# Kernel tuning notes

Measured on AMD Instinct MI355X. Metric: run time of the kernel, lower is better.

Reference implementation:

```python
import jax, jax.numpy as jnp
import numpy as np

EPS = 1e-5  # torch LayerNorm default
H = 8       # heads_num


def _ln(t, g, b):
    m = jnp.mean(t, axis=-1, keepdims=True)
    v = jnp.var(t, axis=-1, keepdims=True)
    return (t - m) / jnp.sqrt(v + EPS) * g + b


def setup_inputs() -> dict:
    key = jax.random.key(0)
    ks = jax.random.split(key, 12)
    B, S, Dq, Dk, Dff = 4, 2048, 512, 768, 2048
    def w(k, shape, scale=0.02):
        return jax.random.normal(k, shape, jnp.float32) * scale
    return {
        "x": jax.random.normal(ks[0], (B, S, Dq), jnp.float32),
        "y": jax.random.normal(ks[1], (B, S, Dk), jnp.float32),
        # cross-attention projections (stored [in, out]; linear_q/k/v have no bias)
        "Wq": w(ks[2], (Dq, Dq)), "Wk": w(ks[3], (Dk, Dq)), "Wv": w(ks[4], (Dk, Dq)),
        "Wo": w(ks[5], (Dq, Dq)), "bo": jnp.zeros((Dq,), jnp.float32),
        # nn.MultiheadAttention packed in-projection and out-projection
        "mha_w_in": w(ks[6], (Dq, 3 * Dq)), "mha_b_in": jnp.zeros((3 * Dq,), jnp.float32),
        "mha_wo": w(ks[7], (Dq, Dq)), "mha_bo": jnp.zeros((Dq,), jnp.float32),
        # 4 LayerNorms
        "ln1_g": jnp.ones((Dq,), jnp.float32), "ln1_b": jnp.zeros((Dq,), jnp.float32),
        "ln2_g": jnp.ones((Dk,), jnp.float32), "ln2_b": jnp.zeros((Dk,), jnp.float32),
        "ln3_g": jnp.ones((Dq,), jnp.float32), "ln3_b": jnp.zeros((Dq,), jnp.float32),
        "ln4_g": jnp.ones((Dq,), jnp.float32), "ln4_b": jnp.zeros((Dq,), jnp.float32),
        # dense MLP (moe=False branch)
        "mlp_w1": w(ks[8], (Dq, Dff)), "mlp_b1": jnp.zeros((Dff,), jnp.float32),
        "mlp_w2": w(ks[9], (Dff, Dq)), "mlp_b2": jnp.zeros((Dq,), jnp.float32),
    }


def reference(x, y, Wq, Wk, Wv, Wo, bo, mha_w_in, mha_b_in, mha_wo, mha_bo,
              ln1_g, ln1_b, ln2_g, ln2_b, ln3_g, ln3_b, ln4_g, ln4_b,
              mlp_w1, mlp_b1, mlp_w2, mlp_b2):
    B, S, D = x.shape
    hd = D // H
    inv_sqrt_hd = 1.0 / np.sqrt(hd).astype(np.float32)

    xn = _ln(x, ln1_g, ln1_b)
    yn = _ln(y, ln2_g, ln2_b)

    # ---- Multi_CrossAttention: manual QK^T softmax V over true seq axis ----
    q = (xn @ Wq).reshape(B, S, H, hd)
    k = (yn @ Wk).reshape(B, -1, H, hd)
    v = (yn @ Wv).reshape(B, -1, H, hd)
    scores = jnp.einsum('bqhd,bkhd->bhqk', q, k) * inv_sqrt_hd  # [B,H,S,S] (512 MB)
    attn = jax.nn.softmax(scores, axis=-1)
    ctx = jnp.einsum('bhqk,bkhd->bqhd', attn, v).reshape(B, S, D)
    ca = ctx @ Wo + bo

    h = _ln(ca + xn, ln3_g, ln3_b)

    # ---- nn.MultiheadAttention (batch_first=False!): axis 0 is the sequence ----
    qkv = h @ mha_w_in + mha_b_in  # [L=B, N=S, 3D]
    q2, k2, v2 = jnp.split(qkv, 3, axis=-1)
    L, N = q2.shape[0], q2.shape[1]
    q2 = q2.reshape(L, N, H, hd)
    k2 = k2.reshape(L, N, H, hd)
    v2 = v2.reshape(L, N, H, hd)
    s2 = jnp.einsum('lnhd,mnhd->nhlm', q2, k2) * inv_sqrt_hd  # [N,H,L,L]
    a2 = jax.nn.softmax(s2, axis=-1)
    sa = jnp.einsum('nhlm,mnhd->lnhd', a2, v2).reshape(L, N, D) @ mha_wo + mha_bo

    h2 = _ln(sa + h, ln4_g, ln4_b)

    # ---- dense MLP (GELU exact, dropout=0) ----
    mlp = jax.nn.gelu(h2 @ mlp_w1 + mlp_b1, approximate=False) @ mlp_w2 + mlp_b2
    return mlp + h2
```

## Files before the change

kernel.cpp:

```cpp
#include <hip/hip_runtime.h>
#include <math.h>

typedef unsigned short u16;
typedef __attribute__((ext_vector_type(8))) short bf8;
typedef __attribute__((ext_vector_type(4))) float f4;
typedef __attribute__((ext_vector_type(4))) unsigned int u32x4;
typedef __attribute__((ext_vector_type(2))) unsigned int u32x2;
typedef __attribute__((ext_vector_type(4))) unsigned short u16x4;
typedef __attribute__((ext_vector_type(8))) unsigned short u16x8;

__device__ __forceinline__ float bf2f(u16 a){
  unsigned u = ((unsigned)a) << 16;
  float f; __builtin_memcpy(&f, &u, 4);
  return f;
}
__device__ __forceinline__ u16 f2bf(float f){
  unsigned u; __builtin_memcpy(&u, &f, 4);
  u += 0x7fffu + ((u >> 16) & 1u);
  return (u16)(u >> 16);
}
__device__ __forceinline__ unsigned packbf(float a, float b){
  unsigned ua, ub;
  __builtin_memcpy(&ua, &a, 4); __builtin_memcpy(&ub, &b, 4);
  ua += 0x8000u; ub += 0x8000u;
  return __builtin_amdgcn_perm(ub, ua, 0x07060302u);
}
__device__ __forceinline__ void gload16(const u16* g, u16* l){
  __builtin_amdgcn_global_load_lds((const __attribute__((address_space(1))) void*)g,
                                   (__attribute__((address_space(3))) void*)l, 16, 0, 0);
}
__device__ __forceinline__ int xcd_swizzle(int orig, int nwg){
  const int qq = nwg >> 3, rr = nwg & 7;
  const int xcd = orig & 7, loc = orig >> 3;
  return (xcd < rr ? xcd * (qq + 1) : rr * (qq + 1) + (xcd - rr) * qq) + loc;
}

__global__ void k_transpose_all(
    const float* __restrict__ Wq, const float* __restrict__ Wk,
    const float* __restrict__ Wv, const float* __restrict__ Wo,
    const float* __restrict__ Win, const float* __restrict__ Wmo,
    const float* __restrict__ W1, const float* __restrict__ W2,
    u16* __restrict__ WqT, u16* __restrict__ WkT, u16* __restrict__ WvT,
    u16* __restrict__ WoT, u16* __restrict__ WinT, u16* __restrict__ WmoT,
    u16* __restrict__ W1T, u16* __restrict__ W2T)
{
  __shared__ float tile[32][33];
  const int tid = blockIdx.x;
  const float* in; u16* out; int R, C, lo;
  if (tid < 1280){
    if (tid < 256)       { in = Wq;  out = WqT;  R = 512; C = 512;  lo = 0; }
    else if (tid < 640)  { in = Wk;  out = WkT;  R = 768; C = 512;  lo = 256; }
    else if (tid < 1024) { in = Wv;  out = WvT;  R = 768; C = 512;  lo = 640; }
    else                 { in = Wo;  out = WoT;  R = 512; C = 512;  lo = 1024; }
  } else {
    if (tid < 2048)      { in = Win; out = WinT; R = 512; C = 1536; lo = 1280; }
    else if (tid < 2304) { in = Wmo; out = WmoT; R = 512; C = 512;  lo = 2048; }
    else if (tid < 3328) { in = W1;  out = W1T;  R = 512; C = 2048; lo = 2304; }
    else                 { in = W2;  out = W2T;  R = 2048; C = 512; lo = 3328; }
  }
  const int local = tid - lo;
  const int tpx = C >> 5;
  const int bx = (local % tpx) * 32, by = (local / tpx) * 32;
  const int tx = threadIdx.x, ty = threadIdx.y;
#pragma unroll
  for (int i = 0; i < 4; i++)
    tile[ty + i*8][tx] = in[(size_t)(by + ty + i*8) * C + bx + tx];
  __syncthreads();
#pragma unroll
  for (int i = 0; i < 4; i++)
    out[(size_t)(bx + ty + i*8) * R + by + tx] = f2bf(tile[tx][ty + i*8]);
}

__global__ __launch_bounds__(256) void k_layernorm(
    const float* __restrict__ in, const float* __restrict__ gam,
    const float* __restrict__ bet, float* __restrict__ outf,
    u16* __restrict__ outb, int D)
{
  const int row = blockIdx.x, t = threadIdx.x;
  const int nv = D >> 8;
  const float* r = in + (size_t)row * D;
  float v[3] = {0.f, 0.f, 0.f};
  float s = 0.f, s2 = 0.f;
#pragma unroll
  for (int i = 0; i < 3; i++){
    if (i < nv){ float xx = r[t + i*256]; v[i] = xx; s += xx; s2 += xx*xx; }
  }
#pragma unroll
  for (int m = 32; m; m >>= 1){ s += __shfl_xor(s, m); s2 += __shfl_xor(s2, m); }
  __shared__ float rs[4], rq[4];
  const int wave = t >> 6;
  if ((t & 63) == 0){ rs[wave] = s; rq[wave] = s2; }
  __syncthreads();
  s  = rs[0] + rs[1] + rs[2] + rs[3];
  s2 = rq[0] + rq[1] + rq[2] + rq[3];
  const float mean = s / (float)D;
  const float var  = s2 / (float)D - mean * mean;
  const float rstd = rsqrtf(var + 1e-5f);
#pragma unroll
  for (int i = 0; i < 3; i++){
    if (i < nv){
      const int c = t + i*256;
      float o = (v[i] - mean) * rstd * gam[c] + bet[c];
      if (outf) outf[(size_t)row * D + c] = o;
      outb[(size_t)row * D + c] = f2bf(o);
    }
  }
}

template<int TM, int TN, bool BIAS, bool RES, bool GELU_ACT, int OUTM>
__global__ __launch_bounds__(256, 4) void k_gemm(
    const u16* __restrict__ A, const u16* __restrict__ BT,
    const float* __restrict__ bias, const float* __restrict__ res,
    float* __restrict__ outf, u16* __restrict__ outb,
    int M, int N, int K)
{
  constexpr int MF = TM / 32;
  constexpr int NF = TN / 32;
  constexpr int WM = TM / 2;
  constexpr int WN = TN / 2;
  __shared__ u16 Sb[(TM + TN) * 64];
  const int t = threadIdx.x;
  const int gx = gridDim.x;
  const int swz = xcd_swizzle(blockIdx.y * gx + blockIdx.x, gx * gridDim.y);
  const int m0 = (swz / gx) * TM, n0 = (swz % gx) * TN;
  const int wave = t >> 6, lane = t & 63;
  const int wm = wave >> 1, wn = wave & 1;
  const int l15 = lane & 15, lg = lane >> 4;
  const u16* Ag = A + (size_t)m0 * K;
  const u16* Bg = BT + (size_t)n0 * K;

  const int lrow = lane >> 3;
  const int csrc = (((lane & 7) ^ lrow) << 3);
  const u16* Agl = Ag + (size_t)lrow * K + csrc;
  const u16* Bgl = Bg + (size_t)lrow * K + csrc;

  f4 acc[MF][NF];
#pragma unroll
  for (int i = 0; i < MF; i++)
#pragma unroll
    for (int j = 0; j < NF; j++) acc[i][j] = (f4){0.f, 0.f, 0.f, 0.f};

  const int nK = K >> 6;
#pragma unroll
  for (int i = 0; i < TM/32; i++){
    const int rb = (i*4 + wave) * 8;
    gload16(Agl + (size_t)rb * K, &Sb[rb * 64]);
  }
#pragma unroll
  for (int i = 0; i < TN/32; i++){
    const int rb = (i*4 + wave) * 8;
    gload16(Bgl + (size_t)rb * K, &Sb[(TM + rb) * 64]);
  }
  asm volatile("s_waitcnt vmcnt(0)" ::: "memory");
  __syncthreads();

  for (int kt = 0;; kt++){
    const char* As = (const char*)&Sb[0];
    const char* Bs = (const char*)&Sb[TM * 64];
#pragma unroll
    for (int kc = 0; kc < 2; kc++){
      bf8 af[MF], bfr[NF];
      const int kb = kc*64 + lg*16;
#pragma unroll
      for (int mf = 0; mf < MF; mf++){
        const int row = wm*WM + mf*16 + l15;
        af[mf] = *(const bf8*)(As + row*128 + (kb ^ ((row & 7) << 4)));
      }
#pragma unroll
      for (int nf = 0; nf < NF; nf++){
        const int row = wn*WN + nf*16 + l15;
        bfr[nf] = *(const bf8*)(Bs + row*128 + (kb ^ ((row & 7) << 4)));
      }
#pragma unroll
      for (int mf = 0; mf < MF; mf++)
#pragma unroll
        for (int nf = 0; nf < NF; nf++)
          acc[mf][nf] = __builtin_amdgcn_mfma_f32_16x16x32_bf16(af[mf], bfr[nf], acc[mf][nf], 0, 0, 0);
    }
    if (kt + 1 == nK) break;
    __syncthreads();
    const int ko = (kt + 1) << 6;
#pragma unroll
    for (int i = 0; i < TM/32; i++){
      const int rb = (i*4 + wave) * 8;
      gload16(Agl + (size_t)rb * K + ko, &Sb[rb * 64]);
    }
#pragma unroll
    for (int i = 0; i < TN/32; i++){
      const int rb = (i*4 + wave) * 8;
      gload16(Bgl + (size_t)rb * K + ko, &Sb[(TM + rb) * 64]);
    }
    asm volatile("s_waitcnt vmcnt(0)" ::: "memory");
    __syncthreads();
  }
#pragma unroll
  for (int mf = 0; mf < MF; mf++){
#pragma unroll
    for (int nf = 0; nf < NF; nf++){
      const int colg = n0 + wn*WN + nf*16 + l15;
      const int rowg = m0 + wm*WM + mf*16 + lg*4;
      const float bv = BIAS ? bias[colg] : 0.f;
      float vv[4];
#pragma unroll
      for (int j = 0; j < 4; j++){
        float v = acc[mf][nf][j] + bv;
        if (RES) v += res[(size_t)(rowg + j) * N + colg];
        if (GELU_ACT) v = 0.5f * v * (1.f + erff(v * 0.7071067811865475f));
        vv[j] = v;
      }
      if (OUTM == 0){
#pragma unroll
        for (int j = 0; j < 4; j++) outf[(size_t)(rowg + j) * N + colg] = vv[j];
      } else if (OUTM == 1){
#pragma unroll
        for (int j = 0; j < 4; j++) outb[(size_t)(rowg + j) * N + colg] = f2bf(vv[j]);
      } else {
        const int bb = rowg >> 11, ss = rowg & 2047;
        u16x4 pk;
#pragma unroll
        for (int j = 0; j < 4; j++) pk[j] = f2bf(vv[j]);
        *(u16x4*)(outb + ((size_t)(bb*512 + colg)) * 2048 + ss) = pk;
      }
    }
  }
}

__global__ __launch_bounds__(256, 2) void k_flash(
    const u16* __restrict__ q, const u16* __restrict__ k,
    const u16* __restrict__ vt, u16* __restrict__ ctx)
{
  __shared__ char Kb[2][64 * 128];
  __shared__ char Vb[2][64 * 128];
  __shared__ char Pb[4][32 * 128];
  const int t = threadIdx.x;
  const int wave = t >> 6, lane = t & 63;
  const int l15 = lane & 15, lg = lane >> 4;
  const int qb = blockIdx.x, bh = blockIdx.y;
  const int b = bh >> 3, h = bh & 7;
  const int qrow0 = qb*128 + wave*32;
  constexpr float CEXP = 0.125f * 1.44269504f;

  bf8 qf[2][2];
#pragma unroll
  for (int qg = 0; qg < 2; qg++){
    const u16* qp = q + ((size_t)(b*2048 + qrow0 + qg*16 + l15)) * 512 + h*64 + lg*8;
    qf[qg][0] = *(const bf8*)qp;
    qf[qg][1] = *(const bf8*)(qp + 32);
  }

  const int srow = t >> 3;
  const int sw0  = srow*128 + ((((t & 7) << 4)) ^ ((srow & 7) << 4));
  const u16* kg = k  + ((size_t)(b*2048 + srow)) * 512  + h*64 + ((t & 7) << 3);
  const u16* vg = vt + ((size_t)(b*512 + h*64 + srow)) * 2048 + ((t & 7) << 3);

  u32x4 rk0 = *(const u32x4*)kg;
  u32x4 rk1 = *(const u32x4*)(kg + 32*512);
  u32x4 rv0 = *(const u32x4*)vg;
  u32x4 rv1 = *(const u32x4*)(vg + 32*2048);
  *(u32x4*)(Kb[0] + sw0)          = rk0;
  *(u32x4*)(Kb[0] + sw0 + 32*128) = rk1;
  *(u32x4*)(Vb[0] + sw0)          = rv0;
  *(u32x4*)(Vb[0] + sw0 + 32*128) = rv1;

  f4 o[2][4];
#pragma unroll
  for (int qg = 0; qg < 2; qg++)
#pragma unroll
    for (int nb = 0; nb < 4; nb++) o[qg][nb] = (f4){0.f,0.f,0.f,0.f};
  float rl[2] = {0.f, 0.f};
  char* myp = Pb[wave];
  const int psw = (l15 & 7) << 4;

  int cur = 0;
  for (int it = 0; it < 32; it++){
    __syncthreads();
    if (it + 1 < 32){
      const size_t kt = (size_t)(it + 1) << 6;
      rk0 = *(const u32x4*)(kg + kt*512);
      rk1 = *(const u32x4*)(kg + kt*512 + 32*512);
      rv0 = *(const u32x4*)(vg + kt);
      rv1 = *(const u32x4*)(vg + kt + 32*2048);
    }
    const char* kbuf = Kb[cur];
    const char* vbuf = Vb[cur];
    f4 s[4][2];
    __builtin_amdgcn_s_setprio(1);
#pragma unroll
    for (int nb = 0; nb < 4; nb++){
      const int row = nb*16 + l15;
      const int sx = (row & 7) << 4;
      const bf8 kf0 = *(const bf8*)(kbuf + row*128 + ((lg*16) ^ sx));
      const bf8 kf1 = *(const bf8*)(kbuf + row*128 + ((64 + lg*16) ^ sx));
#pragma unroll
      for (int qg = 0; qg < 2; qg++){
        f4 a = (f4){0.f,0.f,0.f,0.f};
        a = __builtin_amdgcn_mfma_f32_16x16x32_bf16(kf0, qf[qg][0], a, 0, 0, 0);
        a = __builtin_amdgcn_mfma_f32_16x16x32_bf16(kf1, qf[qg][1], a, 0, 0, 0);
        s[nb][qg] = a;
      }
    }
    __builtin_amdgcn_s_setprio(0);
#pragma unroll
    for (int qg = 0; qg < 2; qg++){
      float p[4][4];
#pragma unroll
      for (int nb = 0; nb < 4; nb++)
#pragma unroll
        for (int j = 0; j < 4; j++)
          p[nb][j] = __builtin_amdgcn_exp2f(s[nb][qg][j] * CEXP);
      float ts = ((p[0][0]+p[1][0]) + (p[2][0]+p[3][0]))
               + ((p[0][1]+p[1][1]) + (p[2][1]+p[3][1]))
               + ((p[0][2]+p[1][2]) + (p[2][2]+p[3][2]))
               + ((p[0][3]+p[1][3]) + (p[2][3]+p[3][3]));
      ts += __shfl_xor(ts, 16);
      ts += __shfl_xor(ts, 32);
      rl[qg] += ts;
#pragma unroll
      for (int nb = 0; nb < 4; nb++){
        u32x2 w;
        w[0] = packbf(p[nb][0], p[nb][1]);
        w[1] = packbf(p[nb][2], p[nb][3]);
        *(u32x2*)(myp + (qg*16 + l15)*128 + ((nb*32 + lg*8) ^ psw)) = w;
      }
    }
    asm volatile("s_waitcnt lgkmcnt(0)" ::: "memory");
    __builtin_amdgcn_sched_barrier(0);
    bf8 pf[2][2], vf[4][2];
#pragma unroll
    for (int qg = 0; qg < 2; qg++){
      const int pr = (qg*16 + l15)*128;
      pf[qg][0] = *(const bf8*)(myp + pr + ((lg*16) ^ psw));
      pf[qg][1] = *(const bf8*)(myp + pr + ((64 + lg*16) ^ psw));
    }
#pragma unroll
    for (int nb = 0; nb < 4; nb++){
      const int row = nb*16 + l15;
      const int sx = (row & 7) << 4;
      vf[nb][0] = *(const bf8*)(vbuf + row*128 + ((lg*16) ^ sx));
      vf[nb][1] = *(const bf8*)(vbuf + row*128 + ((64 + lg*16) ^ sx));
    }
    __builtin_amdgcn_s_setprio(1);
#pragma unroll
    for (int nb = 0; nb < 4; nb++)
#pragma unroll
      for (int qg = 0; qg < 2; qg++){
        o[qg][nb] = __builtin_amdgcn_mfma_f32_16x16x32_bf16(pf[qg][0], vf[nb][0], o[qg][nb], 0, 0, 0);
        o[qg][nb] = __builtin_amdgcn_mfma_f32_16x16x32_bf16(pf[qg][1], vf[nb][1], o[qg][nb], 0, 0, 0);
      }
    __builtin_amdgcn_s_setprio(0);
    __syncthreads();
    if (it + 1 < 32){
      char* kb2 = Kb[cur ^ 1];
      char* vb2 = Vb[cur ^ 1];
      *(u32x4*)(kb2 + sw0)          = rk0;
      *(u32x4*)(kb2 + sw0 + 32*128) = rk1;
      *(u32x4*)(vb2 + sw0)          = rv0;
      *(u32x4*)(vb2 + sw0 + 32*128) = rv1;
      cur ^= 1;
    }
  }
#pragma unroll
  for (int qg = 0; qg < 2; qg++){
    const float i0 = 1.f / __shfl(rl[qg], lg*4 + 0);
    const float i1 = 1.f / __shfl(rl[qg], lg*4 + 1);
    const float i2 = 1.f / __shfl(rl[qg], lg*4 + 2);
    const float i3 = 1.f / __shfl(rl[qg], lg*4 + 3);
#pragma unroll
    for (int nb = 0; nb < 4; nb++){
      u16* cp = ctx + ((size_t)(b*2048 + qrow0 + qg*16 + lg*4)) * 512 + h*64 + nb*16 + l15;
      cp[0]    = f2bf(o[qg][nb][0] * i0);
      cp[512]  = f2bf(o[qg][nb][1] * i1);
      cp[1024] = f2bf(o[qg][nb][2] * i2);
      cp[1536] = f2bf(o[qg][nb][3] * i3);
    }
  }
}

__global__ __launch_bounds__(256) void k_mha_small(const u16* __restrict__ qkv,
                                                   u16* __restrict__ outb)
{
  const int tid = blockIdx.x * 256 + threadIdx.x;
  const int n = tid & 2047;
  const int hl = tid >> 11;
  const int h = hl >> 2, l = hl & 3;
  const u16* qp = qkv + ((size_t)l * 2048 + n) * 1536 + h*64;
  float qv[64];
#pragma unroll
  for (int i = 0; i < 8; i++){
    const bf8 c = *(const bf8*)(qp + i*8);
#pragma unroll
    for (int j2 = 0; j2 < 8; j2++) qv[i*8 + j2] = bf2f((u16)c[j2]) * 0.125f;
  }
  float sc[4];
#pragma unroll
  for (int m = 0; m < 4; m++){
    const u16* kp = qkv + ((size_t)m * 2048 + n) * 1536 + 512 + h*64;
    float a = 0.f;
#pragma unroll
    for (int i = 0; i < 8; i++){
      const bf8 c = *(const bf8*)(kp + i*8);
#pragma unroll
      for (int j2 = 0; j2 < 8; j2++) a += qv[i*8 + j2] * bf2f((u16)c[j2]);
    }
    sc[m] = a;
  }
  const float mx = fmaxf(fmaxf(sc[0], sc[1]), fmaxf(sc[2], sc[3]));
  float p[4]; float sum = 0.f;
#pragma unroll
  for (int m = 0; m < 4; m++){ p[m] = __expf(sc[m] - mx); sum += p[m]; }
  const float inv = 1.f / sum;
  float ov[64];
#pragma unroll
  for (int i = 0; i < 64; i++) ov[i] = 0.f;
#pragma unroll
  for (int m = 0; m < 4; m++){
    const float pw = p[m] * inv;
    const u16* vp = qkv + ((size_t)m * 2048 + n) * 1536 + 1024 + h*64;
#pragma unroll
    for (int i = 0; i < 8; i++){
      const bf8 c = *(const bf8*)(vp + i*8);
#pragma unroll
      for (int j2 = 0; j2 < 8; j2++) ov[i*8 + j2] += pw * bf2f((u16)c[j2]);
    }
  }
  u16* op = outb + ((size_t)l * 2048 + n) * 512 + h*64;
#pragma unroll
  for (int i = 0; i < 8; i++){
    u16x8 pk;
#pragma unroll
    for (int j2 = 0; j2 < 8; j2++) pk[j2] = f2bf(ov[i*8 + j2]);
    *(u16x8*)(op + i*8) = pk;
  }
}

extern "C" void kernel_launch(void* const* d_in, const int* in_sizes, int n_in,
                              void* d_out, int out_size, void* d_ws, size_t ws_size,
                              hipStream_t stream)
{
  (void)in_sizes; (void)n_in; (void)out_size; (void)ws_size;
  const float* x    = (const float*)d_in[0];
  const float* y    = (const float*)d_in[1];
  const float* Wq   = (const float*)d_in[2];
  const float* Wk   = (const float*)d_in[3];
  const float* Wv   = (const float*)d_in[4];
  const float* Wo   = (const float*)d_in[5];
  const float* bo   = (const float*)d_in[6];
  const float* Win  = (const float*)d_in[7];
  const float* bin  = (const float*)d_in[8];
  const float* Wmo  = (const float*)d_in[9];
  const float* bmo  = (const float*)d_in[10];
  const float* ln1g = (const float*)d_in[11];
  const float* ln1b = (const float*)d_in[12];
  const float* ln2g = (const float*)d_in[13];
  const float* ln2b = (const float*)d_in[14];
  const float* ln3g = (const float*)d_in[15];
  const float* ln3b = (const float*)d_in[16];
  const float* ln4g = (const float*)d_in[17];
  const float* ln4b = (const float*)d_in[18];
  const float* W1   = (const float*)d_in[19];
  const float* b1   = (const float*)d_in[20];
  const float* W2   = (const float*)d_in[21];
  const float* b2   = (const float*)d_in[22];

  char* ws = (char*)d_ws;
  const size_t MB = 1024 * 1024;
  u16* WqT  = (u16*)ws;
  u16* WkT  = WqT  + 512 * 512;
  u16* WvT  = WkT  + 512 * 768;
  u16* WoT  = WvT  + 512 * 768;
  u16* WinT = WoT  + 512 * 512;
  u16* WmoT = WinT + 1536 * 512;
  u16* W1T  = WmoT + 512 * 512;
  u16* W2T  = W1T  + 2048 * 512;
  float* hF   = (float*)(ws + 9 * MB);
  float* xnF  = (float*)(ws + 25 * MB);
  float* carF = (float*)(ws + 41 * MB);
  u16* xnB  = (u16*)(ws + 57 * MB);
  u16* ynB  = (u16*)(ws + 65 * MB);
  u16* qB   = (u16*)(ws + 77 * MB);
  u16* kB   = (u16*)(ws + 85 * MB);
  u16* vtB  = (u16*)(ws + 93 * MB);
  u16* ctxB = (u16*)(ws + 101 * MB);
  float* sarF = xnF;
  float* h2F  = carF;
  u16* saB   = xnB;
  u16* hB    = ynB;
  u16* h2B   = qB;
  u16* qkvB  = kB;
  u16* t1B   = (u16*)hF;

  k_transpose_all<<<4352, dim3(32, 8), 0, stream>>>(
      Wq, Wk, Wv, Wo, Win, Wmo, W1, W2,
      WqT, WkT, WvT, WoT, WinT, WmoT, W1T, W2T);

  k_layernorm<<<8192, 256, 0, stream>>>(x, ln1g, ln1b, xnF, xnB, 512);
  k_layernorm<<<8192, 256, 0, stream>>>(y, ln2g, ln2b, (float*)nullptr, ynB, 768);

  k_gemm<64,128,false,false,false,1><<<dim3(4, 128), 256, 0, stream>>>(xnB, WqT, nullptr, nullptr, nullptr, qB,  8192, 512, 512);
  k_gemm<64,128,false,false,false,1><<<dim3(4, 128), 256, 0, stream>>>(ynB, WkT, nullptr, nullptr, nullptr, kB,  8192, 512, 768);
  k_gemm<64,128,false,false,false,2><<<dim3(4, 128), 256, 0, stream>>>(ynB, WvT, nullptr, nullptr, nullptr, vtB, 8192, 512, 768);

  k_flash<<<dim3(16, 32), 256, 0, stream>>>(qB, kB, vtB, ctxB);

  k_gemm<64,128,true,true,false,0><<<dim3(4, 128), 256, 0, stream>>>(ctxB, WoT, bo, xnF, carF, nullptr, 8192, 512, 512);
  k_layernorm<<<8192, 256, 0, stream>>>(carF, ln3g, ln3b, hF, hB, 512);

  k_gemm<128,128,true,false,false,1><<<dim3(12, 64), 256, 0, stream>>>(hB, WinT, bin, nullptr, nullptr, qkvB, 8192, 1536, 512);
  k_mha_small<<<256, 256, 0, stream>>>(qkvB, saB);
  k_gemm<64,128,true,true,false,0><<<dim3(4, 128), 256, 0, stream>>>(saB, WmoT, bmo, hF, sarF, nullptr, 8192, 512, 512);
  k_layernorm<<<8192, 256, 0, stream>>>(sarF, ln4g, ln4b, h2F, h2B, 512);

  k_gemm<128,128,true,false,true,1><<<dim3(16, 64), 256, 0, stream>>>(h2B, W1T, b1, nullptr, nullptr, t1B, 8192, 2048, 512);
  k_gemm<64,128,true,true,false,0><<<dim3(4, 128), 256, 0, stream>>>(t1B, W2T, b2, h2F, (float*)d_out, nullptr, 8192, 512, 2048);
}
```

Before: 253.1 us.

## Shrink flash-attention query tile, add XCD swizzle, fuse first two layernorms

The flash attention kernel now gives each wave 16 query rows instead of 32, so the grid doubles to 1024 blocks and occupancy rises (launch bounds 4). Block IDs are remapped with an XCD swizzle so blocks sharing K/V land on the same die. The two input layernorms are merged into one launch. In exchange, each K/V tile loaded into LDS is reused by fewer query rows, so K/V traffic per unit of work doubles.

Measured after the change: 247.0 us. 2.4% less time.

```diff
diff --git a/kernel.cpp b/kernel.cpp
--- a/kernel.cpp
+++ b/kernel.cpp
@@ -71,14 +71,12 @@
     out[(size_t)(bx + ty + i*8) * R + by + tx] = f2bf(tile[tx][ty + i*8]);
 }
 
-__global__ __launch_bounds__(256) void k_layernorm(
-    const float* __restrict__ in, const float* __restrict__ gam,
+__device__ __forceinline__ void ln_row(
+    const float* __restrict__ r, const float* __restrict__ gam,
     const float* __restrict__ bet, float* __restrict__ outf,
-    u16* __restrict__ outb, int D)
-{
-  const int row = blockIdx.x, t = threadIdx.x;
+    u16* __restrict__ outb, int D, int t)
+{
   const int nv = D >> 8;
-  const float* r = in + (size_t)row * D;
   float v[3] = {0.f, 0.f, 0.f};
   float s = 0.f, s2 = 0.f;
 #pragma unroll
@@ -101,9 +99,37 @@
     if (i < nv){
       const int c = t + i*256;
       float o = (v[i] - mean) * rstd * gam[c] + bet[c];
-      if (outf) outf[(size_t)row * D + c] = o;
-      outb[(size_t)row * D + c] = f2bf(o);
-    }
+      if (outf) outf[c] = o;
+      outb[c] = f2bf(o);
+    }
+  }
+}
+
+__global__ __launch_bounds__(256) void k_layernorm(
+    const float* __restrict__ in, const float* __restrict__ gam,
+    const float* __restrict__ bet, float* __restrict__ outf,
+    u16* __restrict__ outb, int D)
+{
+  const int row = blockIdx.x;
+  ln_row(in + (size_t)row * D, gam, bet,
+         outf ? outf + (size_t)row * D : nullptr,
+         outb + (size_t)row * D, D, threadIdx.x);
+}
+
+__global__ __launch_bounds__(256) void k_layernorm12(
+    const float* __restrict__ x, const float* __restrict__ y,
+    const float* __restrict__ g1, const float* __restrict__ b1,
+    const float* __restrict__ g2, const float* __restrict__ b2,
+    float* __restrict__ xnF, u16* __restrict__ xnB, u16* __restrict__ ynB)
+{
+  const int row = blockIdx.x;
+  if (row < 8192){
+    ln_row(x + (size_t)row * 512, g1, b1, xnF + (size_t)row * 512,
+           xnB + (size_t)row * 512, 512, threadIdx.x);
+  } else {
+    const int r2 = row - 8192;
+    ln_row(y + (size_t)r2 * 768, g2, b2, nullptr,
+           ynB + (size_t)r2 * 768, 768, threadIdx.x);
   }
 }
 
@@ -225,28 +251,26 @@
   }
 }
 
-__global__ __launch_bounds__(256, 2) void k_flash(
+__global__ __launch_bounds__(256, 4) void k_flash(
     const u16* __restrict__ q, const u16* __restrict__ k,
     const u16* __restrict__ vt, u16* __restrict__ ctx)
 {
   __shared__ char Kb[2][64 * 128];
   __shared__ char Vb[2][64 * 128];
-  __shared__ char Pb[4][32 * 128];
+  __shared__ char Pb[4][16 * 128];
   const int t = threadIdx.x;
   const int wave = t >> 6, lane = t & 63;
   const int l15 = lane & 15, lg = lane >> 4;
-  const int qb = blockIdx.x, bh = blockIdx.y;
+  const int id = blockIdx.y * 32 + blockIdx.x;
+  const int swz = xcd_swizzle(id, 1024);
+  const int qb = swz & 31, bh = swz >> 5;
   const int b = bh >> 3, h = bh & 7;
-  const int qrow0 = qb*128 + wave*32;
+  const int qrow0 = qb*64 + wave*16;
   constexpr float CEXP = 0.125f * 1.44269504f;
 
-  bf8 qf[2][2];
-#pragma unroll
-  for (int qg = 0; qg < 2; qg++){
-    const u16* qp = q + ((size_t)(b*2048 + qrow0 + qg*16 + l15)) * 512 + h*64 + lg*8;
-    qf[qg][0] = *(const bf8*)qp;
-    qf[qg][1] = *(const bf8*)(qp + 32);
-  }
+  const u16* qp = q + ((size_t)(b*2048 + qrow0 + l15)) * 512 + h*64 + lg*8;
+  const bf8 qf0 = *(const bf8*)qp;
+  const bf8 qf1 = *(const bf8*)(qp + 32);
 
   const int srow = t >> 3;
   const int sw0  = srow*128 + ((((t & 7) << 4)) ^ ((srow & 7) << 4));
@@ -262,12 +286,10 @@
   *(u32x4*)(Vb[0] + sw0)          = rv0;
   *(u32x4*)(Vb[0] + sw0 + 32*128) = rv1;
 
-  f4 o[2][4];
-#pragma unroll
-  for (int qg = 0; qg < 2; qg++)
-#pragma unroll
-    for (int nb = 0; nb < 4; nb++) o[qg][nb] = (f4){0.f,0.f,0.f,0.f};
-  float rl[2] = {0.f, 0.f};
+  f4 o[4];
+#pragma unroll
+  for (int nb = 0; nb < 4; nb++) o[nb] = (f4){0.f,0.f,0.f,0.f};
+  float rl = 0.f;
   char* myp = Pb[wave];
   const int psw = (l15 & 7) << 4;
 
@@ -283,7 +305,7 @@
     }
     const char* kbuf = Kb[cur];
     const char* vbuf = Vb[cur];
-    f4 s[4][2];
+    f4 s[4];
     __builtin_amdgcn_s_setprio(1);
 #pragma unroll
     for (int nb = 0; nb < 4; nb++){
@@ -291,47 +313,37 @@
       const int sx = (row & 7) << 4;
       const bf8 kf0 = *(const bf8*)(kbuf + row*128 + ((lg*16) ^ sx));
       const bf8 kf1 = *(const bf8*)(kbuf + row*128 + ((64 + lg*16) ^ sx));
-#pragma unroll
-      for (int qg = 0; qg < 2; qg++){
-        f4 a = (f4){0.f,0.f,0.f,0.f};
-        a = __builtin_amdgcn_mfma_f32_16x16x32_bf16(kf0, qf[qg][0], a, 0, 0, 0);
-        a = __builtin_amdgcn_mfma_f32_16x16x32_bf16(kf1, qf[qg][1], a, 0, 0, 0);
-        s[nb][qg] = a;
-      }
+      f4 a = (f4){0.f,0.f,0.f,0.f};
+      a = __builtin_amdgcn_mfma_f32_16x16x32_bf16(kf0, qf0, a, 0, 0, 0);
+      a = __builtin_amdgcn_mfma_f32_16x16x32_bf16(kf1, qf1, a, 0, 0, 0);
+      s[nb] = a;
     }
     __builtin_amdgcn_s_setprio(0);
-#pragma unroll
-    for (int qg = 0; qg < 2; qg++){
-      float p[4][4];
-#pragma unroll
-      for (int nb = 0; nb < 4; nb++)
-#pragma unroll
-        for (int j = 0; j < 4; j++)
-          p[nb][j] = __builtin_amdgcn_exp2f(s[nb][qg][j] * CEXP);
-      float ts = ((p[0][0]+p[1][0]) + (p[2][0]+p[3][0]))
-               + ((p[0][1]+p[1][1]) + (p[2][1]+p[3][1]))
-               + ((p[0][2]+p[1][2]) + (p[2][2]+p[3][2]))
-               + ((p[0][3]+p[1][3]) + (p[2][3]+p[3][3]));
-      ts += __shfl_xor(ts, 16);
-      ts += __shfl_xor(ts, 32);
-      rl[qg] += ts;
-#pragma unroll
-      for (int nb = 0; nb < 4; nb++){
-        u32x2 w;
-        w[0] = packbf(p[nb][0], p[nb][1]);
-        w[1] = packbf(p[nb][2], p[nb][3]);
-        *(u32x2*)(myp + (qg*16 + l15)*128 + ((nb*32 + lg*8) ^ psw)) = w;
-      }
+    float p[4][4];
+#pragma unroll
+    for (int nb = 0; nb < 4; nb++)
+#pragma unroll
+      for (int j = 0; j < 4; j++)
+        p[nb][j] = __builtin_amdgcn_exp2f(s[nb][j] * CEXP);
+    float ts = ((p[0][0]+p[1][0]) + (p[2][0]+p[3][0]))
+             + ((p[0][1]+p[1][1]) + (p[2][1]+p[3][1]))
+             + ((p[0][2]+p[1][2]) + (p[2][2]+p[3][2]))
+             + ((p[0][3]+p[1][3]) + (p[2][3]+p[3][3]));
+    ts += __shfl_xor(ts, 16);
+    ts += __shfl_xor(ts, 32);
+    rl += ts;
+#pragma unroll
+    for (int nb = 0; nb < 4; nb++){
+      u32x2 w;
+      w[0] = packbf(p[nb][0], p[nb][1]);
+      w[1] = packbf(p[nb][2], p[nb][3]);
+      *(u32x2*)(myp + l15*128 + ((nb*32 + lg*8) ^ psw)) = w;
     }
     asm volatile("s_waitcnt lgkmcnt(0)" ::: "memory");
     __builtin_amdgcn_sched_barrier(0);
-    bf8 pf[2][2], vf[4][2];
-#pragma unroll
-    for (int qg = 0; qg < 2; qg++){
-      const int pr = (qg*16 + l15)*128;
-      pf[qg][0] = *(const bf8*)(myp + pr + ((lg*16) ^ psw));
-      pf[qg][1] = *(const bf8*)(myp + pr + ((64 + lg*16) ^ psw));
-    }
+    const bf8 pf0 = *(const bf8*)(myp + l15*128 + ((lg*16) ^ psw));
+    const bf8 pf1 = *(const bf8*)(myp + l15*128 + ((64 + lg*16) ^ psw));
+    bf8 vf[4][2];
 #pragma unroll
     for (int nb = 0; nb < 4; nb++){
       const int row = nb*16 + l15;
@@ -341,12 +353,10 @@
     }
     __builtin_amdgcn_s_setprio(1);
 #pragma unroll
-    for (int nb = 0; nb < 4; nb++)
-#pragma unroll
-      for (int qg = 0; qg < 2; qg++){
-        o[qg][nb] = __builtin_amdgcn_mfma_f32_16x16x32_bf16(pf[qg][0], vf[nb][0], o[qg][nb], 0, 0, 0);
-        o[qg][nb] = __builtin_amdgcn_mfma_f32_16x16x32_bf16(pf[qg][1], vf[nb][1], o[qg][nb], 0, 0, 0);
-      }
+    for (int nb = 0; nb < 4; nb++){
+      o[nb] = __builtin_amdgcn_mfma_f32_16x16x32_bf16(pf0, vf[nb][0], o[nb], 0, 0, 0);
+      o[nb] = __builtin_amdgcn_mfma_f32_16x16x32_bf16(pf1, vf[nb][1], o[nb], 0, 0, 0);
+    }
     __builtin_amdgcn_s_setprio(0);
     __syncthreads();
     if (it + 1 < 32){
@@ -359,20 +369,17 @@
       cur ^= 1;
     }
   }
-#pragma unroll
-  for (int qg = 0; qg < 2; qg++){
-    const float i0 = 1.f / __shfl(rl[qg], lg*4 + 0);
-    const float i1 = 1.f / __shfl(rl[qg], lg*4 + 1);
-    const float i2 = 1.f / __shfl(rl[qg], lg*4 + 2);
-    const float i3 = 1.f / __shfl(rl[qg], lg*4 + 3);
-#pragma unroll
-    for (int nb = 0; nb < 4; nb++){
-      u16* cp = ctx + ((size_t)(b*2048 + qrow0 + qg*16 + lg*4)) * 512 + h*64 + nb*16 + l15;
-      cp[0]    = f2bf(o[qg][nb][0] * i0);
-      cp[512]  = f2bf(o[qg][nb][1] * i1);
-      cp[1024] = f2bf(o[qg][nb][2] * i2);
-      cp[1536] = f2bf(o[qg][nb][3] * i3);
-    }
+  const float i0 = 1.f / __shfl(rl, lg*4 + 0);
+  const float i1 = 1.f / __shfl(rl, lg*4 + 1);
+  const float i2 = 1.f / __shfl(rl, lg*4 + 2);
+  const float i3 = 1.f / __shfl(rl, lg*4 + 3);
+#pragma unroll
+  for (int nb = 0; nb < 4; nb++){
+    u16* cp = ctx + ((size_t)(b*2048 + qrow0 + lg*4)) * 512 + h*64 + nb*16 + l15;
+    cp[0]    = f2bf(o[nb][0] * i0);
+    cp[512]  = f2bf(o[nb][1] * i1);
+    cp[1024] = f2bf(o[nb][2] * i2);
+    cp[1536] = f2bf(o[nb][3] * i3);
   }
 }
 
@@ -493,14 +500,14 @@
       Wq, Wk, Wv, Wo, Win, Wmo, W1, W2,
       WqT, WkT, WvT, WoT, WinT, WmoT, W1T, W2T);
 
-  k_layernorm<<<8192, 256, 0, stream>>>(x, ln1g, ln1b, xnF, xnB, 512);
-  k_layernorm<<<8192, 256, 0, stream>>>(y, ln2g, ln2b, (float*)nullptr, ynB, 768);
+  k_layernorm12<<<16384, 256, 0, stream>>>(x, y, ln1g, ln1b, ln2g, ln2b,
+                                           xnF, xnB, ynB);
 
   k_gemm<64,128,false,false,false,1><<<dim3(4, 128), 256, 0, stream>>>(xnB, WqT, nullptr, nullptr, nullptr, qB,  8192, 512, 512);
   k_gemm<64,128,false,false,false,1><<<dim3(4, 128), 256, 0, stream>>>(ynB, WkT, nullptr, nullptr, nullptr, kB,  8192, 512, 768);
   k_gemm<64,128,false,false,false,2><<<dim3(4, 128), 256, 0, stream>>>(ynB, WvT, nullptr, nullptr, nullptr, vtB, 8192, 512, 768);
 
-  k_flash<<<dim3(16, 32), 256, 0, stream>>>(qB, kB, vtB, ctxB);
+  k_flash<<<dim3(32, 32), 256, 0, stream>>>(qB, kB, vtB, ctxB);
 
   k_gemm<64,128,true,true,false,0><<<dim3(4, 128), 256, 0, stream>>>(ctxB, WoT, bo, xnF, carF, nullptr, 8192, 512, 512);
   k_layernorm<<<8192, 256, 0, stream>>>(carF, ln3g, ln3b, hF, hB, 512);
```
